# Kernel optimization log

Hardware: AMD Instinct MI355X
Metric: run time of the kernel (lower is better)

Reference implementation:

```python
import jax, jax.numpy as jnp
import numpy as np

EPS = 1e-5

def _ln(x, g, b):
    m = jnp.mean(x, axis=-1, keepdims=True)
    v = jnp.mean((x - m) ** 2, axis=-1, keepdims=True)
    return (x - m) * jax.lax.rsqrt(v + EPS) * g + b

def setup_inputs() -> dict:
    key = jax.random.key(0)
    B, T, V, D = 32, 512, 16, 128
    ks = jax.random.split(key, 22)
    rn = lambda k, shp, sc: jax.random.normal(k, shp, jnp.float32) * sc
    inp = {
        "x": rn(ks[0], (B, T, V), 1.0),
        # per-variable GRN params (stacked over the V variables)
        "W1": rn(ks[1], (V, D), 1.0),          # fc1: Linear(1, D) weight per var
        "b1": rn(ks[2], (V, D), 0.02),
        "W2": rn(ks[3], (V, D, D), 1.0 / np.sqrt(D)),   # fc2: Linear(D, D)
        "b2": rn(ks[4], (V, D), 0.02),
        "Wg": rn(ks[5], (V, D, D), 1.0 / np.sqrt(D)),   # gate: Linear(D, D)
        "bg": rn(ks[6], (V, D), 0.02),
        "Ws": rn(ks[7], (V, D), 1.0),          # skip: Linear(1, D)
        "bs": rn(ks[8], (V, D), 0.02),
        "gamma": jnp.ones((V, D), jnp.float32),
        "beta": jnp.zeros((V, D), jnp.float32),
        # softmax GRN params: d_in = V*D, d_hidden = D, d_out = V
        "sW1": rn(ks[9], (D, V * D), 1.0 / np.sqrt(V * D)),
        "sb1": rn(ks[10], (D,), 0.02),
        "sW2": rn(ks[11], (V, D), 1.0 / np.sqrt(D)),
        "sb2": rn(ks[12], (V,), 0.02),
        "sWg": rn(ks[13], (V, D), 1.0 / np.sqrt(D)),
        "sbg": rn(ks[14], (V,), 0.02),
        "sWs": rn(ks[15], (V, V * D), 1.0 / np.sqrt(V * D)),
        "sbs": rn(ks[16], (V,), 0.02),
        "sgamma": jnp.ones((V,), jnp.float32),
        "sbeta": jnp.zeros((V,), jnp.float32),
    }
    return inp

def reference(x, W1, b1, W2, b2, Wg, bg, Ws, bs, gamma, beta,
              sW1, sb1, sW2, sb2, sWg, sbg, sWs, sbs, sgamma, sbeta):
    V, D = W1.shape
    lead = x.shape[:-1]
    xf = x.reshape(-1, V)                                  # (N, V)
    # ---- all per-variable GRNs batched over the var dim ----
    h = jax.nn.elu(xf[..., None] * W1 + b1)                # (N, V, D)
    h2 = jnp.einsum('nvd,vod->nvo', h, W2) + b2            # (N, V, D)
    g = jax.nn.sigmoid(jnp.einsum('nvd,vod->nvo', h, Wg) + bg)
    skip = xf[..., None] * Ws + bs                         # (N, V, D)
    stacked = _ln(g * h2 + (1.0 - g) * skip, gamma, beta)  # (N, V, D)
    # ---- softmax GRN over flattened embeddings ----
    flat = stacked.reshape(-1, V * D)                      # (N, V*D)
    hs = jax.nn.elu(flat @ sW1.T + sb1)                    # (N, D)
    h2s = hs @ sW2.T + sb2                                 # (N, V)
    gs = jax.nn.sigmoid(hs @ sWg.T + sbg)
    sks = flat @ sWs.T + sbs
    weights = jax.nn.softmax(_ln(gs * h2s + (1.0 - gs) * sks, sgamma, sbeta), axis=-1)
    processed = jnp.einsum('nvd,nv->nd', stacked, weights) # (N, D)
    return processed.reshape(*lead, D), weights.reshape(*lead, V)
```

## Files before the change

kernel.cpp:

```cpp
#include <hip/hip_runtime.h>
#include <hip/hip_bf16.h>
#include <math.h>

#define NVAR 16
#define ND 128
#define NVD 2048
#define NROWS 16384
#define RTA 256
#define NRB 32

typedef short s16x8 __attribute__((ext_vector_type(8)));
typedef short s16x4 __attribute__((ext_vector_type(4)));
typedef float f32x4 __attribute__((ext_vector_type(4)));
typedef unsigned short u16;

#define MFMA(a,b,c) __builtin_amdgcn_mfma_f32_16x16x32_bf16((a),(b),(c),0,0,0)

#define OFF_W2  0
#define OFF_WG  262144
#define OFF_SW1 524288
#define OFF_SWS 786432
#define OFF_SW2 819200
#define OFF_SWG 821248
#define WS_ELEMS 823296
#define OFF_STK 823296
#define STK_ELEMS ((size_t)NROWS*NVD)
#define WS_NEEDED_BYTES (((size_t)WS_ELEMS + STK_ELEMS)*2)
#define SV_ELEMS ((size_t)(NROWS/16)*2048)

__device__ __forceinline__ unsigned f2bf(float f){
    union { float f; unsigned u; } c; c.f = f;
    unsigned u = c.u;
    u += 0x7fffu + ((u >> 16) & 1u);
    return u >> 16;
}
__device__ __forceinline__ float bf2f(unsigned bits){
    union { unsigned u; float f; } c; c.u = bits << 16;
    return c.f;
}
__device__ __forceinline__ float eluf(float x){ return x > 0.f ? x : __expf(x) - 1.f; }
__device__ __forceinline__ float sigm(float x){
    return __builtin_amdgcn_rcpf(1.f + __expf(-x));
}

__device__ __forceinline__ int offHs(int r, int c){
    return r*128 + ((((c>>3) ^ (r&7))<<3) | (c&7));
}
__device__ __forceinline__ int offBig(int r, int c){
    return r*2048 + ((((c>>3) ^ (r&7))<<3) | (c&7));
}

__global__ void prep_kernel(const float* __restrict__ W2, const float* __restrict__ Wg,
                            const float* __restrict__ sW1, const float* __restrict__ sWs,
                            const float* __restrict__ sW2, const float* __restrict__ sWg,
                            u16* __restrict__ ws){
    int i = blockIdx.x*256 + threadIdx.x;
    if (i >= WS_ELEMS) return;
    float v;
    if      (i < OFF_WG)  v = W2[i];
    else if (i < OFF_SW1) v = Wg[i-OFF_WG];
    else if (i < OFF_SWS) v = sW1[i-OFF_SW1];
    else if (i < OFF_SW2) v = sWs[i-OFF_SWS];
    else if (i < OFF_SWG) v = sW2[i-OFF_SW2];
    else                  v = sWg[i-OFF_SWG];
    ws[i] = (u16)f2bf(v);
}

__global__ __launch_bounds__(512, 2)
void vsn_varA(const float* __restrict__ x,
              const float* __restrict__ W1, const float* __restrict__ b1,
              const float* __restrict__ b2, const float* __restrict__ bg,
              const float* __restrict__ Wsk, const float* __restrict__ bsk,
              const float* __restrict__ gamma, const float* __restrict__ beta,
              u16* __restrict__ ws)
{
    __shared__ u16 lw2[128*128];
    __shared__ u16 lwg[128*128];
    __shared__ float lp[8*128];
    __shared__ float lxv[RTA];

    const int t = threadIdx.x, w = t>>6, l = t&63;
    const int hr = l>>4, c16 = l&15;
    const int v = blockIdx.y;
    const int row0 = blockIdx.x*RTA;

    #pragma unroll
    for (int i=0;i<8;++i){
        int cid = i*512 + t;
        int mat = cid>>11, within = cid&2047;
        int r = within>>4, c8 = within&15;
        const u16* src = ws + (mat? OFF_WG:OFF_W2) + v*16384 + r*128 + c8*8;
        s16x8 val = *reinterpret_cast<const s16x8*>(src);
        u16* dst = (mat? lwg:lw2) + r*128 + ((c8 ^ (r&7))<<3);
        *reinterpret_cast<s16x8*>(dst) = val;
    }
    if (t < 128){
        lp[t]     = W1[v*ND+t];    lp[128+t] = b1[v*ND+t];
        lp[256+t] = b2[v*ND+t];    lp[384+t] = bg[v*ND+t];
        lp[512+t] = Wsk[v*ND+t];   lp[640+t] = bsk[v*ND+t];
        lp[768+t] = gamma[v*ND+t]; lp[896+t] = beta[v*ND+t];
    }
    if (t < RTA) lxv[t] = x[(size_t)(row0+t)*NVAR + v];
    __syncthreads();

    #pragma unroll 1
    for (int pass=0; pass<2; ++pass){
        const int lrow0 = (w + pass*8)*16;
        const float xv = lxv[lrow0 + c16];

        s16x8 B[4];
        #pragma unroll
        for (int ks=0;ks<4;++ks){
            s16x8 o;
            #pragma unroll
            for (int j=0;j<8;++j){
                int c = ks*32 + hr*8 + j;
                o[j] = (short)f2bf(eluf(xv*lp[c] + lp[128+c]));
            }
            B[ks] = o;
        }
        __builtin_amdgcn_sched_barrier(0);

        float y[8][4];
        #pragma unroll
        for (int ct=0; ct<8; ++ct){
            f32x4 a2 = {0.f,0.f,0.f,0.f}, ag = {0.f,0.f,0.f,0.f};
            const int wr = ct*16 + c16;
            #pragma unroll
            for (int ks=0;ks<4;++ks){
                int chunk = (ks*4 + hr) ^ (wr&7);
                s16x8 A2 = *reinterpret_cast<const s16x8*>(lw2 + wr*128 + chunk*8);
                a2 = MFMA(A2, B[ks], a2);
            }
            #pragma unroll
            for (int ks=0;ks<4;++ks){
                int chunk = (ks*4 + hr) ^ (wr&7);
                s16x8 Ag = *reinterpret_cast<const s16x8*>(lwg + wr*128 + chunk*8);
                ag = MFMA(Ag, B[ks], ag);
            }
            const int obb = ct*16 + hr*4;
            float4 b2v = *reinterpret_cast<const float4*>(&lp[256+obb]);
            float4 bgv = *reinterpret_cast<const float4*>(&lp[384+obb]);
            float4 wsv = *reinterpret_cast<const float4*>(&lp[512+obb]);
            float4 bsv = *reinterpret_cast<const float4*>(&lp[640+obb]);
            #pragma unroll
            for (int j=0;j<4;++j){
                float h2 = a2[j] + reinterpret_cast<const float*>(&b2v)[j];
                float gg = sigm(ag[j] + reinterpret_cast<const float*>(&bgv)[j]);
                float sk = xv*reinterpret_cast<const float*>(&wsv)[j]
                           + reinterpret_cast<const float*>(&bsv)[j];
                y[ct][j] = gg*h2 + (1.f-gg)*sk;
            }
            __builtin_amdgcn_sched_barrier(0);
        }
        float s = 0.f, q = 0.f;
        #pragma unroll
        for (int ct=0;ct<8;++ct)
            #pragma unroll
            for (int j=0;j<4;++j){ float yy = y[ct][j]; s += yy; q += yy*yy; }
        s += __shfl_xor(s, 16); s += __shfl_xor(s, 32);
        q += __shfl_xor(q, 16); q += __shfl_xor(q, 32);
        float mean = s*(1.f/ND);
        float inv  = rsqrtf(q*(1.f/ND) - mean*mean + 1e-5f);

        const int grp = blockIdx.x*16 + w + pass*8;
        u16* stkb = ws + OFF_STK + (size_t)v*SV_ELEMS + (size_t)grp*2048;
        #pragma unroll
        for (int ctp=0; ctp<4; ++ctp){
            s16x8 o;
            #pragma unroll
            for (int hh=0; hh<2; ++hh){
                int ct = ctp*2 + hh;
                const int obb = ct*16 + hr*4;
                float4 gm = *reinterpret_cast<const float4*>(&lp[768+obb]);
                float4 bt = *reinterpret_cast<const float4*>(&lp[896+obb]);
                #pragma unroll
                for (int j=0;j<4;++j){
                    float z = (y[ct][j]-mean)*inv*reinterpret_cast<const float*>(&gm)[j]
                              + reinterpret_cast<const float*>(&bt)[j];
                    o[hh*4+j] = (short)f2bf(z);
                }
            }
            *reinterpret_cast<s16x8*>(stkb + ctp*512 + c16*32 + hr*8) = o;
            __builtin_amdgcn_sched_barrier(0);
        }
    }
}

__device__ __forceinline__ s16x8 ldA(const u16* abuf, int vrel, int rg, int ctp, int n, int hr){
    int base = (((vrel*2 + rg)*4 + ctp)*16 + n)*32;
    int fn = (n>>1)&3;
    int u0 = (hr&1)*2;
    int half = (hr>>1)*4;
    s16x4 lo = *reinterpret_cast<const s16x4*>(abuf + base + (((u0  )^fn)<<3) + half);
    s16x4 hi = *reinterpret_cast<const s16x4*>(abuf + base + (((u0+1)^fn)<<3) + half);
    s16x8 r;
    r[0]=lo[0]; r[1]=lo[1]; r[2]=lo[2]; r[3]=lo[3];
    r[4]=hi[0]; r[5]=hi[1]; r[6]=hi[2]; r[7]=hi[3];
    return r;
}

__global__ __launch_bounds__(512, 4)
void vsn_softB(const u16* __restrict__ ws,
               const float* __restrict__ sb1, const float* __restrict__ sb2,
               const float* __restrict__ sbg, const float* __restrict__ sbs,
               const float* __restrict__ sgamma, const float* __restrict__ sbeta,
               float* __restrict__ out_proc, float* __restrict__ out_w)
{
    __shared__ u16   abuf[8192];
    __shared__ u16   hsb[32*128];
    __shared__ float pps_[4*32*16];
    __shared__ float pph[32*16];
    __shared__ float ppg[32*16];
    __shared__ float sksf[32*16];
    __shared__ float wgtb[32*16];

    float* pps = pps_;

    const int t = threadIdx.x, w = t>>6, l = t&63;
    const int hr = l>>4, c16 = l&15;
    const int row0 = blockIdx.x * NRB;
    const int grp0 = row0 >> 4;
    const int orow = w*16 + c16;
    const int rgs = w & 1;
    const int khf = w >> 1;

    const u16* stk  = ws + OFF_STK;
    const u16* sW1b = ws + OFF_SW1;
    const u16* sWsb = ws + OFF_SWS;

    f32x4 accHs[2] = {{0,0,0,0},{0,0,0,0}};
    f32x4 accSk = {0,0,0,0};

    #pragma unroll 1
    for (int kt=0; kt<8; ++kt){
        #pragma unroll
        for (int i=0;i<2;++i){
            int cid = i*512 + t;
            int vv  = kt*2 + (cid>>9);
            int rg  = (cid>>8)&1;
            int n   = (cid>>2)&15;
            int u   = cid&3;
            const u16* src = stk + (size_t)vv*SV_ELEMS + (size_t)(grp0+rg)*2048
                           + ((cid>>2)&63)*32 + u*8;
            s16x8 val = *reinterpret_cast<const s16x8*>(src);
            *reinterpret_cast<s16x8*>(abuf + (cid>>2)*32 + ((u ^ ((n>>1)&3))<<3)) = val;
        }
        __syncthreads();
        #pragma unroll
        for (int ks=0; ks<8; ++ks){
            s16x8 bf = *reinterpret_cast<const s16x8*>(
                sW1b + (size_t)orow*NVD + kt*256 + ks*32 + hr*8);
            #pragma unroll
            for (int rg=0; rg<2; ++rg){
                s16x8 af = ldA(abuf, ks>>2, rg, ks&3, c16, hr);
                accHs[rg] = MFMA(af, bf, accHs[rg]);
            }
        }
        #pragma unroll
        for (int kk=0; kk<2; ++kk){
            int ks = khf*2 + kk;
            s16x8 bf = *reinterpret_cast<const s16x8*>(
                sWsb + (size_t)c16*NVD + kt*256 + ks*32 + hr*8);
            s16x8 af = ldA(abuf, ks>>2, rgs, ks&3, c16, hr);
            accSk = MFMA(af, bf, accSk);
        }
        __syncthreads();
    }

    {
        float bb = sb1[orow];
        #pragma unroll
        for (int rg=0; rg<2; ++rg){
            #pragma unroll
            for (int j=0;j<4;++j){
                int r = rg*16 + hr*4 + j;
                hsb[offHs(r, orow)] = (u16)f2bf(eluf(accHs[rg][j] + bb));
            }
        }
        #pragma unroll
        for (int j=0;j<4;++j)
            pps[khf*512 + (rgs*16 + hr*4 + j)*16 + c16] = accSk[j];
    }
    __syncthreads();

    sksf[t] = pps[t] + pps[512+t] + pps[1024+t] + pps[1536+t] + sbs[t&15];
    if (w < 4){
        const u16* Bsrc = (w < 2) ? (ws + OFF_SW2) : (ws + OFF_SWG);
        int rg = w & 1;
        f32x4 acc = {0,0,0,0};
        #pragma unroll
        for (int ks=0; ks<4; ++ks){
            int rr = rg*16 + c16;
            int chunk = (ks*4 + hr) ^ (rr&7);
            s16x8 af = *reinterpret_cast<const s16x8*>(hsb + rr*128 + chunk*8);
            s16x8 bf = *reinterpret_cast<const s16x8*>(Bsrc + c16*ND + ks*32 + hr*8);
            acc = MFMA(af, bf, acc);
        }
        float* dst = (w < 2) ? pph : ppg;
        #pragma unroll
        for (int j=0;j<4;++j)
            dst[(rg*16 + hr*4 + j)*16 + c16] = acc[j];
    }
    __syncthreads();

    {
        int r = t>>4, vv = t & 15;
        float h2s = pph[r*16+vv] + sb2[vv];
        float gs  = sigm(ppg[r*16+vv] + sbg[vv]);
        float yv  = gs*h2s + (1.f-gs)*sksf[r*16+vv];
        float ssum = yv, qsum = yv*yv;
        #pragma unroll
        for (int m=1;m<16;m<<=1){ ssum += __shfl_xor(ssum,m,16); qsum += __shfl_xor(qsum,m,16); }
        float mean = ssum*(1.f/NVAR);
        float var  = qsum*(1.f/NVAR) - mean*mean;
        float z = (yv-mean)*rsqrtf(var+1e-5f)*sgamma[vv] + sbeta[vv];
        float mx = z;
        #pragma unroll
        for (int m=1;m<16;m<<=1) mx = fmaxf(mx, __shfl_xor(mx,m,16));
        float e = __expf(z-mx);
        float es = e;
        #pragma unroll
        for (int m=1;m<16;m<<=1) es += __shfl_xor(es,m,16);
        float wgt = e * __builtin_amdgcn_rcpf(es);
        wgtb[r*16+vv] = wgt;
        out_w[(size_t)(row0+r)*NVAR + vv] = wgt;
    }
    __syncthreads();

    {
        int r = t>>4, cu = t&15;
        int ctp = cu>>2, u = cu&3;
        int grp = (row0+r)>>4, n = r&15;
        float acc[8] = {0,0,0,0,0,0,0,0};
        #pragma unroll
        for (int v=0; v<NVAR; ++v){
            float wv = wgtb[r*16 + v];
            const u16* sp = stk + (size_t)v*SV_ELEMS + (size_t)grp*2048
                          + (ctp*16+n)*32 + u*8;
            s16x8 sv = *reinterpret_cast<const s16x8*>(sp);
            #pragma unroll
            for (int k=0;k<8;++k) acc[k] += bf2f((u16)sv[k]) * wv;
        }
        float* op = out_proc + (size_t)(row0+r)*ND + ctp*32 + u*4;
        float4 lo = { acc[0], acc[1], acc[2], acc[3] };
        float4 hi = { acc[4], acc[5], acc[6], acc[7] };
        *reinterpret_cast<float4*>(op)      = lo;
        *reinterpret_cast<float4*>(op + 16) = hi;
    }
}

__global__ __launch_bounds__(512, 4)
void vsn_fused(const float* __restrict__ x,
               const float* __restrict__ W1, const float* __restrict__ b1,
               const float* __restrict__ b2, const float* __restrict__ bg,
               const float* __restrict__ Wsk, const float* __restrict__ bsk,
               const float* __restrict__ gamma, const float* __restrict__ beta,
               const float* __restrict__ sb1, const float* __restrict__ sb2,
               const float* __restrict__ sbg, const float* __restrict__ sbs,
               const float* __restrict__ sgamma, const float* __restrict__ sbeta,
               const u16* __restrict__ ws,
               float* __restrict__ out_proc, float* __restrict__ out_w)
{
    __shared__ u16   big[16*2048];
    __shared__ u16   hsb[16*128];
    __shared__ float pp[8*256];
    __shared__ float psumbuf[256];
    __shared__ float sksbuf[256];
    __shared__ float sx[256];

    float* psum  = psumbuf;
    float* psum2 = psumbuf + 128;

    const int t   = threadIdx.x;
    const int w   = t >> 6;
    const int l   = t & 63;
    const int hr  = l >> 4;
    const int c16 = l & 15;
    const int row0 = blockIdx.x * 16;
    const int orow = w*16 + c16;

    if (t < 256) sx[t] = x[row0*NVAR + t];
    __syncthreads();

    const u16* W2b = ws + OFF_W2;
    const u16* Wgb = ws + OFF_WG;

    for (int v = 0; v < NVAR; ++v){
        #pragma unroll
        for (int i = 0; i < 4; ++i){
            int idx = i*512 + t;
            int r = idx >> 7, d = idx & 127;
            float hv = eluf(sx[r*NVAR+v]*W1[v*ND+d] + b1[v*ND+d]);
            big[offBig(r, v*ND+d)] = (u16)f2bf(hv);
        }
        __syncthreads();

        s16x8 A[4];
        #pragma unroll
        for (int ks = 0; ks < 4; ++ks)
            A[ks] = *reinterpret_cast<const s16x8*>(&big[offBig(c16, v*ND + ks*32 + hr*8)]);
        const s16x8* B2p = reinterpret_cast<const s16x8*>(W2b + v*ND*ND + orow*ND + hr*8);
        const s16x8* Bgp = reinterpret_cast<const s16x8*>(Wgb + v*ND*ND + orow*ND + hr*8);
        f32x4 acc2 = {0.f,0.f,0.f,0.f}, accg = {0.f,0.f,0.f,0.f};
        #pragma unroll
        for (int ks = 0; ks < 4; ++ks) acc2 = MFMA(A[ks], B2p[ks*4], acc2);
        #pragma unroll
        for (int ks = 0; ks < 4; ++ks) accg = MFMA(A[ks], Bgp[ks*4], accg);

        const float b2v = b2[v*ND+orow], bgv = bg[v*ND+orow];
        const float wsv = Wsk[v*ND+orow], bsv = bsk[v*ND+orow];
        float y[4];
        #pragma unroll
        for (int j = 0; j < 4; ++j){
            int r = hr*4 + j;
            float h2 = acc2[j] + b2v;
            float g  = sigm(accg[j] + bgv);
            float sk = sx[r*NVAR+v]*wsv + bsv;
            y[j] = g*h2 + (1.f-g)*sk;
        }
        float s[4], q[4];
        #pragma unroll
        for (int j=0;j<4;++j){ s[j]=y[j]; q[j]=y[j]*y[j]; }
        #pragma unroll
        for (int m=1; m<16; m<<=1){
            #pragma unroll
            for (int j=0;j<4;++j){
                s[j] += __shfl_xor(s[j], m, 16);
                q[j] += __shfl_xor(q[j], m, 16);
            }
        }
        if (c16 == 0){
            #pragma unroll
            for (int j=0;j<4;++j){
                psum [(hr*4+j)*8 + w] = s[j];
                psum2[(hr*4+j)*8 + w] = q[j];
            }
        }
        __syncthreads();

        if (t < 16){
            float ss=0.f, qq=0.f;
            #pragma unroll
            for (int ww=0; ww<8; ++ww){ ss += psum[t*8+ww]; qq += psum2[t*8+ww]; }
            float mean = ss*(1.f/ND);
            float var  = qq*(1.f/ND) - mean*mean;
            sksbuf[t]      = mean;
            sksbuf[16 + t] = rsqrtf(var + 1e-5f);
        }
        __syncthreads();

        const float gm = gamma[v*ND+orow], bt = beta[v*ND+orow];
        #pragma unroll
        for (int j=0;j<4;++j){
            int r = hr*4 + j;
            float z = (y[j]-sksbuf[r])*sksbuf[16+r]*gm + bt;
            big[offBig(r, v*ND+orow)] = (u16)f2bf(z);
        }
    }
    __syncthreads();

    const u16* sW1b = ws + OFF_SW1;
    {
        f32x4 acc0 = {0,0,0,0}, acc1 = {0,0,0,0};
        const s16x8* Bp = reinterpret_cast<const s16x8*>(sW1b + orow*NVD + hr*8);
        #pragma unroll 8
        for (int ks = 0; ks < 64; ks += 2){
            s16x8 A0 = *reinterpret_cast<const s16x8*>(&big[offBig(c16, ks*32 + hr*8)]);
            s16x8 A1 = *reinterpret_cast<const s16x8*>(&big[offBig(c16, (ks+1)*32 + hr*8)]);
            acc0 = MFMA(A0, Bp[ks*4],     acc0);
            acc1 = MFMA(A1, Bp[(ks+1)*4], acc1);
        }
        float bb = sb1[orow];
        #pragma unroll
        for (int j=0;j<4;++j){
            int r = hr*4 + j;
            hsb[offHs(r, orow)] = (u16)f2bf(eluf(acc0[j] + acc1[j] + bb));
        }
    }
    const u16* sWsb = ws + OFF_SWS;
    {
        f32x4 acc = {0,0,0,0};
        const s16x8* Bp = reinterpret_cast<const s16x8*>(sWsb + c16*NVD + hr*8);
        #pragma unroll
        for (int kk = 0; kk < 8; ++kk){
            int ks = w*8 + kk;
            s16x8 Af = *reinterpret_cast<const s16x8*>(&big[offBig(c16, ks*32 + hr*8)]);
            acc = MFMA(Af, Bp[ks*4], acc);
        }
        #pragma unroll
        for (int j=0;j<4;++j)
            pp[w*256 + (hr*4+j)*16 + c16] = acc[j];
    }
    __syncthreads();

    if (t < 256){
        float a = sbs[t & 15];
        #pragma unroll
        for (int ww=0; ww<8; ++ww) a += pp[ww*256 + t];
        sksbuf[t] = a;
    }
    __syncthreads();

    {
        const u16* Bsrc = (w < 4) ? (ws + OFF_SW2) : (ws + OFF_SWG);
        const int m = w & 3;
        s16x8 Af = *reinterpret_cast<const s16x8*>(&hsb[offHs(c16, m*32 + hr*8)]);
        s16x8 Bf = *reinterpret_cast<const s16x8*>(Bsrc + c16*ND + m*32 + hr*8);
        f32x4 z4 = {0,0,0,0};
        f32x4 acc = MFMA(Af, Bf, z4);
        #pragma unroll
        for (int j=0;j<4;++j)
            pp[w*256 + (hr*4+j)*16 + c16] = acc[j];
    }
    __syncthreads();

    if (t < 256){
        int r = t >> 4, vv = t & 15;
        float h2s = sb2[vv], gp = sbg[vv];
        #pragma unroll
        for (int j=0;j<4;++j){ h2s += pp[j*256 + t]; gp += pp[(4+j)*256 + t]; }
        float gs = sigm(gp);
        float yv = gs*h2s + (1.f-gs)*sksbuf[t];
        float ssum = yv, qsum = yv*yv;
        #pragma unroll
        for (int m=1;m<16;m<<=1){ ssum += __shfl_xor(ssum,m,16); qsum += __shfl_xor(qsum,m,16); }
        float mean = ssum*(1.f/NVAR);
        float var  = qsum*(1.f/NVAR) - mean*mean;
        float z = (yv-mean)*rsqrtf(var+1e-5f)*sgamma[vv] + sbeta[vv];
        float mx = z;
        #pragma unroll
        for (int m=1;m<16;m<<=1) mx = fmaxf(mx, __shfl_xor(mx,m,16));
        float e = __expf(z-mx);
        float es = e;
        #pragma unroll
        for (int m=1;m<16;m<<=1) es += __shfl_xor(es,m,16);
        float wgt = e/es;
        psumbuf[t] = wgt;
        out_w[(row0+r)*NVAR + vv] = wgt;
    }
    __syncthreads();

    if (t < 256){
        int r = t >> 4, d8 = (t & 15)*8;
        float acc[8] = {0,0,0,0,0,0,0,0};
        #pragma unroll
        for (int v=0; v<NVAR; ++v){
            float wv = psumbuf[r*NVAR + v];
            s16x8 sv = *reinterpret_cast<const s16x8*>(&big[offBig(r, v*ND + d8)]);
            #pragma unroll
            for (int k=0;k<8;++k) acc[k] += bf2f((u16)sv[k]) * wv;
        }
        float* op = &out_proc[(row0+r)*ND + d8];
        #pragma unroll
        for (int k=0;k<8;++k) op[k] = acc[k];
    }
}

extern "C" void kernel_launch(void* const* d_in, const int* in_sizes, int n_in,
                              void* d_out, int out_size, void* d_ws, size_t ws_size,
                              hipStream_t stream) {
    (void)in_sizes; (void)n_in; (void)out_size;
    const float* x     = (const float*)d_in[0];
    const float* W1    = (const float*)d_in[1];
    const float* b1    = (const float*)d_in[2];
    const float* W2    = (const float*)d_in[3];
    const float* b2    = (const float*)d_in[4];
    const float* Wg    = (const float*)d_in[5];
    const float* bg    = (const float*)d_in[6];
    const float* Wsk   = (const float*)d_in[7];
    const float* bsk   = (const float*)d_in[8];
    const float* gamma = (const float*)d_in[9];
    const float* beta  = (const float*)d_in[10];
    const float* sW1   = (const float*)d_in[11];
    const float* sb1   = (const float*)d_in[12];
    const float* sW2   = (const float*)d_in[13];
    const float* sb2   = (const float*)d_in[14];
    const float* sWg   = (const float*)d_in[15];
    const float* sbg   = (const float*)d_in[16];
    const float* sWs   = (const float*)d_in[17];
    const float* sbs   = (const float*)d_in[18];
    const float* sgam  = (const float*)d_in[19];
    const float* sbet  = (const float*)d_in[20];

    u16* ws = (u16*)d_ws;
    float* out_proc = (float*)d_out;
    float* out_w    = out_proc + (size_t)NROWS * ND;

    prep_kernel<<<(WS_ELEMS + 255)/256, 256, 0, stream>>>(W2, Wg, sW1, sWs, sW2, sWg, ws);

    if (ws_size >= WS_NEEDED_BYTES) {
        vsn_varA<<<dim3(NROWS/RTA, NVAR), 512, 0, stream>>>(
            x, W1, b1, b2, bg, Wsk, bsk, gamma, beta, ws);
        vsn_softB<<<NROWS/NRB, 512, 0, stream>>>(
            ws, sb1, sb2, sbg, sbs, sgam, sbet, out_proc, out_w);
    } else {
        vsn_fused<<<NROWS/16, 512, 0, stream>>>(
            x, W1, b1, b2, bg, Wsk, bsk, gamma, beta,
            sb1, sb2, sbg, sbs, sgam, sbet, ws, out_proc, out_w);
    }
}
```

Measured before the change: 108.8 us.

## Load stacked A fragments directly from global memory instead of staging through LDS

The softmax-GRN GEMM stage no longer cooperatively copies the stacked activations into a swizzled shared-memory buffer each k-tile with two barriers. Each wave now reads its MFMA A fragments straight from global memory (relying on L1/L2 reuse across the eight waves) and folds the skip-projection MFMA into the main ks loop. This removes the LDS staging, the swizzle arithmetic and the per-tile __syncthreads, and frees 16KB of LDS. In exchange, each wave issues redundant global loads of the same data and the skip branch is guarded per wave.

```diff
diff --git a/kernel.cpp b/kernel.cpp
--- a/kernel.cpp
+++ b/kernel.cpp
@@ -187,13 +187,9 @@
     }
 }
 
-__device__ __forceinline__ s16x8 ldA(const u16* abuf, int vrel, int rg, int ctp, int n, int hr){
-    int base = (((vrel*2 + rg)*4 + ctp)*16 + n)*32;
-    int fn = (n>>1)&3;
-    int u0 = (hr&1)*2;
-    int half = (hr>>1)*4;
-    s16x4 lo = *reinterpret_cast<const s16x4*>(abuf + base + (((u0  )^fn)<<3) + half);
-    s16x4 hi = *reinterpret_cast<const s16x4*>(abuf + base + (((u0+1)^fn)<<3) + half);
+__device__ __forceinline__ s16x8 ldAg(const u16* base32, int u0, int half){
+    s16x4 lo = *reinterpret_cast<const s16x4*>(base32 + u0*8 + half);
+    s16x4 hi = *reinterpret_cast<const s16x4*>(base32 + u0*8 + 8 + half);
     s16x8 r;
     r[0]=lo[0]; r[1]=lo[1]; r[2]=lo[2]; r[3]=lo[3];
     r[4]=hi[0]; r[5]=hi[1]; r[6]=hi[2]; r[7]=hi[3];
@@ -207,7 +203,6 @@
                const float* __restrict__ sgamma, const float* __restrict__ sbeta,
                float* __restrict__ out_proc, float* __restrict__ out_w)
 {
-    __shared__ u16   abuf[8192];
     __shared__ u16   hsb[32*128];
     __shared__ float pps_[4*32*16];
     __shared__ float pph[32*16];
@@ -229,43 +224,32 @@
     const u16* sW1b = ws + OFF_SW1;
     const u16* sWsb = ws + OFF_SWS;
 
+    const int u0   = (hr&1)*2;
+    const int half = (hr>>1)*4;
+
     f32x4 accHs[2] = {{0,0,0,0},{0,0,0,0}};
     f32x4 accSk = {0,0,0,0};
 
     #pragma unroll 1
     for (int kt=0; kt<8; ++kt){
         #pragma unroll
-        for (int i=0;i<2;++i){
-            int cid = i*512 + t;
-            int vv  = kt*2 + (cid>>9);
-            int rg  = (cid>>8)&1;
-            int n   = (cid>>2)&15;
-            int u   = cid&3;
-            const u16* src = stk + (size_t)vv*SV_ELEMS + (size_t)(grp0+rg)*2048
-                           + ((cid>>2)&63)*32 + u*8;
-            s16x8 val = *reinterpret_cast<const s16x8*>(src);
-            *reinterpret_cast<s16x8*>(abuf + (cid>>2)*32 + ((u ^ ((n>>1)&3))<<3)) = val;
-        }
-        __syncthreads();
-        #pragma unroll
         for (int ks=0; ks<8; ++ks){
+            const int vv  = kt*2 + (ks>>2);
+            const int ctp = ks&3;
+            const u16* b0 = stk + (size_t)vv*SV_ELEMS + (size_t)grp0*2048
+                          + ctp*512 + c16*32;
+            s16x8 af0 = ldAg(b0, u0, half);
+            s16x8 af1 = ldAg(b0 + 2048, u0, half);
             s16x8 bf = *reinterpret_cast<const s16x8*>(
                 sW1b + (size_t)orow*NVD + kt*256 + ks*32 + hr*8);
-            #pragma unroll
-            for (int rg=0; rg<2; ++rg){
-                s16x8 af = ldA(abuf, ks>>2, rg, ks&3, c16, hr);
-                accHs[rg] = MFMA(af, bf, accHs[rg]);
-            }
-        }
-        #pragma unroll
-        for (int kk=0; kk<2; ++kk){
-            int ks = khf*2 + kk;
-            s16x8 bf = *reinterpret_cast<const s16x8*>(
-                sWsb + (size_t)c16*NVD + kt*256 + ks*32 + hr*8);
-            s16x8 af = ldA(abuf, ks>>2, rgs, ks&3, c16, hr);
-            accSk = MFMA(af, bf, accSk);
-        }
-        __syncthreads();
+            accHs[0] = MFMA(af0, bf, accHs[0]);
+            accHs[1] = MFMA(af1, bf, accHs[1]);
+            if ((ks>>1) == khf){
+                s16x8 bfs = *reinterpret_cast<const s16x8*>(
+                    sWsb + (size_t)c16*NVD + kt*256 + ks*32 + hr*8);
+                accSk = MFMA(rgs ? af1 : af0, bfs, accSk);
+            }
+        }
     }
 
     {
```

Result: slower. 160.3 us (+47.4%).

## Double-buffer stacked-embedding tiles in LDS with register prefetch in softmax GRN kernel

Applied to the files above, without the earlier changes.

The K-loop in the softmax-GRN kernel now uses two LDS buffers. The next tile's global loads are issued into registers before the MFMA work on the current tile, then written to the alternate buffer afterwards. This drops one __syncthreads per iteration and hides global load latency behind the matrix ops. In exchange it doubles abuf LDS usage to 32KB, which may lower occupancy under launch_bounds(512,4), and it adds register pressure for the prefetched vectors.

```diff
diff --git a/kernel.cpp b/kernel.cpp
--- a/kernel.cpp
+++ b/kernel.cpp
@@ -207,7 +207,7 @@
                const float* __restrict__ sgamma, const float* __restrict__ sbeta,
                float* __restrict__ out_proc, float* __restrict__ out_w)
 {
-    __shared__ u16   abuf[8192];
+    __shared__ u16   abuf[2*8192];
     __shared__ u16   hsb[32*128];
     __shared__ float pps_[4*32*16];
     __shared__ float pph[32*16];
@@ -229,31 +229,39 @@
     const u16* sW1b = ws + OFF_SW1;
     const u16* sWsb = ws + OFF_SWS;
 
+    const int cid0 = t, cid1 = 512 + t;
+    const int rg_0 = (cid0>>8)&1, n_0 = (cid0>>2)&15, u_0 = cid0&3;
+    const int rg_1 = (cid1>>8)&1, n_1 = (cid1>>2)&15, u_1 = cid1&3;
+    const size_t src0 = (size_t)(grp0+rg_0)*2048 + (size_t)((cid0>>2)&63)*32 + u_0*8;
+    const size_t src1 = (size_t)(grp0+rg_1)*2048 + (size_t)((cid1>>2)&63)*32 + u_1*8;
+    const int dst0 = (cid0>>2)*32 + ((u_0 ^ ((n_0>>1)&3))<<3);
+    const int dst1 = (cid1>>2)*32 + ((u_1 ^ ((n_1>>1)&3))<<3);
+
     f32x4 accHs[2] = {{0,0,0,0},{0,0,0,0}};
     f32x4 accSk = {0,0,0,0};
 
+    s16x8 stv0 = *reinterpret_cast<const s16x8*>(stk + src0);
+    s16x8 stv1 = *reinterpret_cast<const s16x8*>(stk + SV_ELEMS + src1);
+    *reinterpret_cast<s16x8*>(abuf + dst0) = stv0;
+    *reinterpret_cast<s16x8*>(abuf + dst1) = stv1;
+    int cur = 0;
+
     #pragma unroll 1
     for (int kt=0; kt<8; ++kt){
-        #pragma unroll
-        for (int i=0;i<2;++i){
-            int cid = i*512 + t;
-            int vv  = kt*2 + (cid>>9);
-            int rg  = (cid>>8)&1;
-            int n   = (cid>>2)&15;
-            int u   = cid&3;
-            const u16* src = stk + (size_t)vv*SV_ELEMS + (size_t)(grp0+rg)*2048
-                           + ((cid>>2)&63)*32 + u*8;
-            s16x8 val = *reinterpret_cast<const s16x8*>(src);
-            *reinterpret_cast<s16x8*>(abuf + (cid>>2)*32 + ((u ^ ((n>>1)&3))<<3)) = val;
+        if (kt < 7){
+            stv0 = *reinterpret_cast<const s16x8*>(stk + (size_t)(kt*2+2)*SV_ELEMS + src0);
+            stv1 = *reinterpret_cast<const s16x8*>(stk + (size_t)(kt*2+3)*SV_ELEMS + src1);
         }
         __syncthreads();
+        const u16* abr = abuf + cur*8192;
+
         #pragma unroll
         for (int ks=0; ks<8; ++ks){
             s16x8 bf = *reinterpret_cast<const s16x8*>(
                 sW1b + (size_t)orow*NVD + kt*256 + ks*32 + hr*8);
             #pragma unroll
             for (int rg=0; rg<2; ++rg){
-                s16x8 af = ldA(abuf, ks>>2, rg, ks&3, c16, hr);
+                s16x8 af = ldA(abr, ks>>2, rg, ks&3, c16, hr);
                 accHs[rg] = MFMA(af, bf, accHs[rg]);
             }
         }
@@ -262,10 +270,16 @@
             int ks = khf*2 + kk;
             s16x8 bf = *reinterpret_cast<const s16x8*>(
                 sWsb + (size_t)c16*NVD + kt*256 + ks*32 + hr*8);
-            s16x8 af = ldA(abuf, ks>>2, rgs, ks&3, c16, hr);
+            s16x8 af = ldA(abr, ks>>2, rgs, ks&3, c16, hr);
             accSk = MFMA(af, bf, accSk);
         }
-        __syncthreads();
+
+        if (kt < 7){
+            u16* abw = abuf + (cur^1)*8192;
+            *reinterpret_cast<s16x8*>(abw + dst0) = stv0;
+            *reinterpret_cast<s16x8*>(abw + dst1) = stv1;
+        }
+        cur ^= 1;
     }
 
     {
```

After: 112.8 us. +3.7%, slower.
